# Performance work log

Measured on AMD Instinct MI355X. Metric: run time of the kernel, lower is better.

## Reference

```python
import jax, jax.numpy as jnp
import numpy as np

INNER_R = 1.0  # args.r * 0.5
OUTER_R = 2.0  # args.r
AXIS = jnp.array([[0, 0, 1], [0, 0, -1], [0, 1, 0], [0, -1, 0], [1, 0, 0], [-1, 0, 0]],
                 dtype=jnp.float32).T  # (3, 6)


def _cos2(xyz):
    # squared clipped cosine of each point direction vs 6 axes
    norm = jnp.linalg.norm(xyz, axis=-1)               # (B, N)
    cos = jnp.maximum(xyz @ AXIS, 0.0) / (norm[..., None] + 1e-8)
    return cos * cos, norm                              # (B, N, 6), (B, N)


def aggregate(direction, xyz, inner_r, outer_r):
    B, N, D6 = direction.shape
    D = D6 // 6
    cos, norm = _cos2(xyz)
    dw = 1.0 - (norm ** 2 - inner_r ** 2) / (outer_r ** 2 - inner_r ** 2)
    dw = jnp.where(dw < 0, 0.0, dw)
    dw = jnp.where(norm <= 0, 0.0, dw)
    dw = dw / jnp.sum(dw, axis=-1, keepdims=True)       # normalize over N
    cos = cos * dw[..., None]                           # (B, N, 6)
    d = direction.reshape(B, N, D, 6) * cos[:, :, None, :]
    return d.sum(axis=(1, 3))                           # sum over axes then points -> (B, D)


def disperse(signal, xyz):
    B, N, D6 = signal.shape
    D = D6 // 6
    cos, _ = _cos2(xyz)
    return (signal.reshape(B, N, D, 6) * cos[:, :, None, :]).sum(axis=-1)  # (B, N, D)


def batchnorm(x, gamma, beta, eps=1e-5):
    # training-mode BN over leading (sample) dim, biased variance like torch
    m = jnp.mean(x, axis=0)
    v = jnp.var(x, axis=0)
    return (x - m) / jnp.sqrt(v + eps) * gamma + beta


def setup_inputs() -> dict:
    key = jax.random.key(0)
    ks = jax.random.split(key, 10)
    B, N, DIM, ENC, MID, VL = 64, 2048, 10, 256, 64, 128
    s = 0.05
    p = lambda k, sh: jax.random.normal(k, sh, dtype=jnp.float32) * s
    x = jax.random.uniform(ks[0], (B, N, DIM), dtype=jnp.float32)  # xyz in [0,1) keeps points inside outer radius
    return {
        "x": x,
        "Wc": p(ks[1], (ENC, DIM)), "bc": jnp.zeros((ENC,), jnp.float32),
        "Wdir": p(ks[2], (MID * 6, DIM)),
        "g1": jnp.ones((MID,), jnp.float32), "b1": jnp.zeros((MID,), jnp.float32),
        "Wdir2": p(ks[3], (ENC, MID)),
        "g2": jnp.ones((ENC,), jnp.float32), "b2": jnp.zeros((ENC,), jnp.float32),
        "Wf1": p(ks[4], (VL, ENC)), "bf1": jnp.zeros((VL,), jnp.float32),
        "Wcm": p(ks[5], (MID, VL + 3)), "bcm": jnp.zeros((MID,), jnp.float32),
        "Wdc": p(ks[6], (ENC * 6, VL + 3)),
        "Wm0": p(ks[7], (MID, ENC)),
        "g3": jnp.ones((MID,), jnp.float32), "b3": jnp.zeros((MID,), jnp.float32),
        "Wf2": p(ks[8], (DIM - 3, MID)), "bf2": jnp.zeros((DIM - 3,), jnp.float32),
    }


def reference(x, Wc, bc, Wdir, g1, b1, Wdir2, g2, b2, Wf1, bf1,
              Wcm, bcm, Wdc, Wm0, g3, b3, Wf2, bf2):
    B, N, C = x.shape
    xyz = x[:, :, :3]
    points = x[:, :, 3:]

    # ---- GeoConv (encode) ----
    center_in = jnp.concatenate([points[:, 0, :], xyz[:, 0, :]], axis=-1)
    center = center_in @ Wc.T + bc  # computed but unused (matches torch: last_bn applied to direction only)
    dir_in = jnp.concatenate([points, xyz], axis=-1)     # (B, N, C)
    direction = dir_in @ Wdir.T                          # (B, N, mid*6)
    direction = aggregate(direction, xyz, INNER_R, OUTER_R)  # (B, mid)
    direction = jax.nn.relu(batchnorm(direction, g1, b1))
    direction = direction @ Wdir2.T                      # (B, enc_out)
    enc = jax.nn.relu(batchnorm(direction, g2, b2))
    z = enc @ Wf1.T + bf1                                # (B, vector_length)

    # ---- GeoDeConv (decode) ----
    c_in = jnp.concatenate([z, xyz[:, 0, :]], axis=-1)
    center2 = c_in @ Wcm.T + bcm                         # (B, mid)
    VL = z.shape[-1]
    sig = jnp.concatenate([xyz, jnp.broadcast_to(z[:, None, :], (B, N, VL))], axis=-1)
    sig = sig @ Wdc.T                                    # (B, N, enc_out*6)
    sig = disperse(sig, xyz)                             # (B, N, enc_out)
    sig = sig @ Wm0.T                                    # (B, N, mid)
    sig = sig.at[:, 0, :].set(center2)                   # inject center signal
    sig = jax.nn.relu(batchnorm(sig.reshape(B * N, -1), g3, b3)).reshape(B, N, -1)

    y = jax.nn.sigmoid(sig @ Wf2.T + bf2)                # (B, N, dim-3)
    return y
```

## Files before the change

kernel.cpp:

```cpp
#include <hip/hip_runtime.h>
#include <math.h>

#define BATCH 64
#define NPTS  2048
#define OFF_M    0
#define OFF_T2   4096
#define OFF_GP2  5248
#define OFF_V    8192
#define OFF_WF1T 57344
#define OFF_D2P  90112
#define OFF_C2   114688
#define OFF_U2   118784
#define OFF_MOM  143360

__global__ __launch_bounds__(256) void k_wa(const float* __restrict__ x,
                                            const float* __restrict__ Wm0,
                                            const float* __restrict__ Wdc,
                                            const float* __restrict__ Wf1,
                                            float* __restrict__ ws) {
    __shared__ __attribute__((aligned(16))) float L[61 * 257];
    int blk = blockIdx.x, t = threadIdx.x;
    if (blk < 24) {
        float* wml = L;
        float* pl  = L + 2112;
        int a = blk >> 2, vq = blk & 3;
        int m = t & 63, vg = t >> 6;
        float acc[8];
#pragma unroll
        for (int i = 0; i < 8; ++i) acc[i] = 0.f;
        for (int e0 = 0; e0 < 256; e0 += 32) {
            for (int g = t; g < 2048; g += 256)
                wml[(g >> 5) * 33 + (g & 31)] = Wm0[(g >> 5) * 256 + e0 + (g & 31)];
            for (int g = t; g < 1024; g += 256)
                pl[(g >> 5) * 36 + (g & 31)] =
                    Wdc[((e0 + (g >> 5)) * 6 + a) * 131 + 3 + vq * 32 + (g & 31)];
            __syncthreads();
#pragma unroll
            for (int e = 0; e < 32; ++e) {
                float wv = wml[m * 33 + e];
                const float4* p4 = (const float4*)(pl + e * 36 + vg * 8);
                float4 pa = p4[0], pb = p4[1];
                acc[0] = fmaf(wv, pa.x, acc[0]); acc[1] = fmaf(wv, pa.y, acc[1]);
                acc[2] = fmaf(wv, pa.z, acc[2]); acc[3] = fmaf(wv, pa.w, acc[3]);
                acc[4] = fmaf(wv, pb.x, acc[4]); acc[5] = fmaf(wv, pb.y, acc[5]);
                acc[6] = fmaf(wv, pb.z, acc[6]); acc[7] = fmaf(wv, pb.w, acc[7]);
            }
            __syncthreads();
        }
#pragma unroll
        for (int vv = 0; vv < 8; ++vv)
            ws[OFF_V + (vq * 32 + vg * 8 + vv) * 384 + m * 6 + a] = acc[vv];
    } else if (blk < 42) {
        float* col = L;
        float* red = L + 256;
        int p = blk - 24, a = p / 3, j = p % 3;
        col[t] = Wdc[(t * 6 + a) * 131 + j];
        __syncthreads();
        int m = t >> 2, q = t & 3;
        const float* wm = Wm0 + m * 256 + q * 64;
        const float* cl = col + q * 64;
        float s = 0.f;
#pragma unroll 8
        for (int i = 0; i < 64; ++i) s = fmaf(wm[i], cl[i], s);
        red[t] = s;
        __syncthreads();
        if (t < 64) {
            float v = (red[t * 4] + red[t * 4 + 1]) + (red[t * 4 + 2] + red[t * 4 + 3]);
            ws[OFF_T2 + t * 18 + a * 3 + j] = v;
        }
    } else if (blk < 106) {
        int b = blk - 42;
        float* red = L;
        float acc[61];
#pragma unroll
        for (int i = 0; i < 61; ++i) acc[i] = 0.f;
#pragma unroll 2
        for (int k = 0; k < 8; ++k) {
            int n = t + 256 * k;
            const float* xp = x + (size_t)(b * NPTS + n) * 10;
            float xv[10];
#pragma unroll
            for (int j = 0; j < 5; ++j) {
                float2 v = *(const float2*)(xp + 2 * j);
                xv[2 * j] = v.x; xv[2 * j + 1] = v.y;
            }
            float x0 = xv[0], x1 = xv[1], x2 = xv[2];
            float rn = x0 * x0 + x1 * x1 + x2 * x2;
            float norm = sqrtf(rn);
            float inv = 1.f / (norm + 1e-8f);
            float c2[6];
            c2[0] = fmaxf(x2, 0.f) * inv; c2[1] = fmaxf(-x2, 0.f) * inv;
            c2[2] = fmaxf(x1, 0.f) * inv; c2[3] = fmaxf(-x1, 0.f) * inv;
            c2[4] = fmaxf(x0, 0.f) * inv; c2[5] = fmaxf(-x0, 0.f) * inv;
#pragma unroll
            for (int a = 0; a < 6; ++a) c2[a] *= c2[a];
            float dw = 1.f - (rn - 1.f) * (1.f / 3.f);
            if (dw < 0.f) dw = 0.f;
            if (norm <= 0.f) dw = 0.f;
            float cw[6];
#pragma unroll
            for (int a = 0; a < 6; ++a) cw[a] = c2[a] * dw;
#pragma unroll
            for (int c = 0; c < 10; ++c) {
                float dv = (c < 7) ? xv[3 + c] : xv[c - 7];
#pragma unroll
                for (int a = 0; a < 6; ++a)
                    acc[c * 6 + a] = fmaf(dv, cw[a], acc[c * 6 + a]);
            }
            acc[60] += dw;
        }
#pragma unroll
        for (int i = 0; i < 61; ++i) red[i * 257 + t] = acc[i];
        __syncthreads();
        if (t < 61) {
            float s = 0.f;
#pragma unroll 8
            for (int j = 0; j < 256; ++j) s += red[t * 257 + j];
            ws[OFF_M + b * 61 + t] = s;
        }
    } else if (blk == 106) {
        if (t < 128) ws[OFF_GP2 + t] = 0.f;
    } else if (blk < 115) {
        float* slab = L;
        int w = blk - 107, v0 = w * 16;
        for (int g = t; g < 4096; g += 256)
            slab[(g >> 8) * 257 + (g & 255)] = Wf1[(v0 + (g >> 8)) * 256 + (g & 255)];
        __syncthreads();
        for (int g = t; g < 4096; g += 256) {
            int e = g >> 4, vl = g & 15;
            ws[OFF_WF1T + e * 128 + v0 + vl] = slab[vl * 257 + e];
        }
    } else if (blk < 179) {
        int b = blk - 115;
        float* red = L;
        float acc[126];
#pragma unroll
        for (int i = 0; i < 126; ++i) acc[i] = 0.f;
        for (int k = 0; k < 8; ++k) {
            int n = t + 256 * k;
            const float* xp = x + (size_t)(b * NPTS + n) * 10;
            float x0 = xp[0], x1 = xp[1], x2 = xp[2];
            float rn = x0 * x0 + x1 * x1 + x2 * x2;
            float inv = 1.f / (sqrtf(rn) + 1e-8f);
            float c[6];
            c[0] = fmaxf(x2, 0.f) * inv; c[1] = fmaxf(-x2, 0.f) * inv;
            c[2] = fmaxf(x1, 0.f) * inv; c[3] = fmaxf(-x1, 0.f) * inv;
            c[4] = fmaxf(x0, 0.f) * inv; c[5] = fmaxf(-x0, 0.f) * inv;
#pragma unroll
            for (int a = 0; a < 6; ++a) c[a] *= c[a];
            float xx[6] = {x0 * x0, x0 * x1, x0 * x2, x1 * x1, x1 * x2, x2 * x2};
#pragma unroll
            for (int a = 0; a < 6; ++a)
#pragma unroll
                for (int a2 = a; a2 < 6; ++a2) {
                    int p = a * 6 - (a * (a - 1)) / 2 + (a2 - a);
                    float cc = c[a] * c[a2];
#pragma unroll
                    for (int q = 0; q < 6; ++q)
                        acc[p * 6 + q] = fmaf(cc, xx[q], acc[p * 6 + q]);
                }
        }
#pragma unroll
        for (int i = 0; i < 61; ++i) red[i * 257 + t] = acc[i];
        __syncthreads();
        if (t < 61) {
            float s = 0.f;
#pragma unroll 8
            for (int j = 0; j < 256; ++j) s += red[t * 257 + j];
            ws[OFF_MOM + b * 240 + 108 + t] = s;
        }
        __syncthreads();
#pragma unroll
        for (int i = 0; i < 61; ++i) red[i * 257 + t] = acc[61 + i];
        __syncthreads();
        if (t < 61) {
            float s = 0.f;
#pragma unroll 8
            for (int j = 0; j < 256; ++j) s += red[t * 257 + j];
            ws[OFF_MOM + b * 240 + 108 + 61 + t] = s;
        }
        __syncthreads();
#pragma unroll
        for (int i = 0; i < 4; ++i) red[i * 257 + t] = acc[122 + i];
        __syncthreads();
        if (t < 4) {
            float s = 0.f;
#pragma unroll 8
            for (int j = 0; j < 256; ++j) s += red[t * 257 + j];
            ws[OFF_MOM + b * 240 + 108 + 122 + t] = s;
        }
    } else {
        int b = blk - 179;
        float* red = L;
        float acc[108];
#pragma unroll
        for (int i = 0; i < 108; ++i) acc[i] = 0.f;
        for (int k = 0; k < 8; ++k) {
            int n = t + 256 * k;
            const float* xp = x + (size_t)(b * NPTS + n) * 10;
            float x0 = xp[0], x1 = xp[1], x2 = xp[2];
            float rn = x0 * x0 + x1 * x1 + x2 * x2;
            float inv = 1.f / (sqrtf(rn) + 1e-8f);
            float c[6];
            c[0] = fmaxf(x2, 0.f) * inv; c[1] = fmaxf(-x2, 0.f) * inv;
            c[2] = fmaxf(x1, 0.f) * inv; c[3] = fmaxf(-x1, 0.f) * inv;
            c[4] = fmaxf(x0, 0.f) * inv; c[5] = fmaxf(-x0, 0.f) * inv;
#pragma unroll
            for (int a = 0; a < 6; ++a) c[a] *= c[a];
#pragma unroll
            for (int a = 0; a < 6; ++a) {
                acc[a] += c[a];
                acc[6 + a * 3 + 0] = fmaf(c[a], x0, acc[6 + a * 3 + 0]);
                acc[6 + a * 3 + 1] = fmaf(c[a], x1, acc[6 + a * 3 + 1]);
                acc[6 + a * 3 + 2] = fmaf(c[a], x2, acc[6 + a * 3 + 2]);
            }
#pragma unroll
            for (int a = 0; a < 6; ++a)
#pragma unroll
                for (int a2 = a; a2 < 6; ++a2) {
                    int p = a * 6 - (a * (a - 1)) / 2 + (a2 - a);
                    float cc = c[a] * c[a2];
                    acc[24 + p] += cc;
                    acc[45 + p * 3 + 0] = fmaf(cc, x0, acc[45 + p * 3 + 0]);
                    acc[45 + p * 3 + 1] = fmaf(cc, x1, acc[45 + p * 3 + 1]);
                    acc[45 + p * 3 + 2] = fmaf(cc, x2, acc[45 + p * 3 + 2]);
                }
        }
#pragma unroll
        for (int i = 0; i < 61; ++i) red[i * 257 + t] = acc[i];
        __syncthreads();
        if (t < 61) {
            float s = 0.f;
#pragma unroll 8
            for (int j = 0; j < 256; ++j) s += red[t * 257 + j];
            ws[OFF_MOM + b * 240 + t] = s;
        }
        __syncthreads();
#pragma unroll
        for (int i = 0; i < 47; ++i) red[i * 257 + t] = acc[61 + i];
        __syncthreads();
        if (t < 47) {
            float s = 0.f;
#pragma unroll 8
            for (int j = 0; j < 256; ++j) s += red[t * 257 + j];
            ws[OFF_MOM + b * 240 + 61 + t] = s;
        }
    }
}

__global__ __launch_bounds__(256) void k_d2(const float* __restrict__ Wdir,
                                            const float* __restrict__ g1,
                                            const float* __restrict__ b1,
                                            const float* __restrict__ Wdir2,
                                            const float* __restrict__ g2,
                                            const float* __restrict__ b2,
                                            float* __restrict__ ws) {
    __shared__ float L[12704];
    float* Wd  = L;
    float* Ml  = L + 3904;
    float* h1  = L + 7808;
    float* wt2 = L + 11968;
    float* d2l = L + 12228;
    float* sc  = L + 12548;
    float* of  = L + 12612;
    float* scl = L + 12676;
    float* ofl = L + 12680;
    int blk = blockIdx.x, t = threadIdx.x;
    int e_base = blk * 4;
    for (int g = t; g < 64 * 61; g += 256) Ml[g] = ws[OFF_M + g];
    for (int g = t; g < 3840; g += 256) Wd[(g / 60) * 61 + g % 60] = Wdir[g];
    if (t < 256) {
        int el = t >> 6, mm = t & 63;
        wt2[el * 65 + mm] = Wdir2[(e_base + el) * 64 + mm];
    }
    __syncthreads();
    int m = t & 63;
    float Wr[60];
#pragma unroll
    for (int r = 0; r < 60; ++r) Wr[r] = Wd[m * 61 + r];
#pragma unroll
    for (int k = 0; k < 16; ++k) {
        int idx = t + 256 * k;
        int b = idx >> 6;
        const float* Mb = Ml + b * 61;
        float s = 0.f;
#pragma unroll
        for (int a = 0; a < 6; ++a)
#pragma unroll
            for (int c = 0; c < 10; ++c)
                s = fmaf(Wr[a * 10 + c], Mb[c * 6 + a], s);
        h1[b * 65 + m] = s / Mb[60];
    }
    __syncthreads();
    if (t < 64) {
        float s = 0.f, q = 0.f;
#pragma unroll 8
        for (int b = 0; b < 64; ++b) { float v = h1[b * 65 + t]; s += v; q = fmaf(v, v, q); }
        float mean = s * (1.f / 64.f);
        float var = q * (1.f / 64.f) - mean * mean;
        float scale = g1[t] * rsqrtf(var + 1e-5f);
        sc[t] = scale; of[t] = b1[t] - mean * scale;
    }
    __syncthreads();
#pragma unroll
    for (int k = 0; k < 16; ++k) {
        int idx = t + 256 * k;
        int b = idx >> 6;
        h1[b * 65 + m] = fmaxf(fmaf(h1[b * 65 + m], sc[m], of[m]), 0.f);
    }
    __syncthreads();
    {
        int b = t >> 2, el = t & 3;
        const float* h = h1 + b * 65;
        const float* w = wt2 + el * 65;
        float s = 0.f;
#pragma unroll
        for (int mm = 0; mm < 64; ++mm) s = fmaf(h[mm], w[mm], s);
        d2l[b * 5 + el] = s;
    }
    __syncthreads();
    if (t < 4) {
        float s = 0.f, q = 0.f;
#pragma unroll 8
        for (int b = 0; b < 64; ++b) { float v = d2l[b * 5 + t]; s += v; q = fmaf(v, v, q); }
        float mean = s * (1.f / 64.f);
        float var = q * (1.f / 64.f) - mean * mean;
        int E = e_base + t;
        float scale = g2[E] * rsqrtf(var + 1e-5f);
        scl[t] = scale; ofl[t] = b2[E] - mean * scale;
    }
    __syncthreads();
    {
        int b = t >> 2, el = t & 3;
        float v = fmaxf(fmaf(d2l[b * 5 + el], scl[el], ofl[el]), 0.f);
        ws[OFF_D2P + b * 256 + e_base + el] = v;
    }
}

__global__ __launch_bounds__(512) void k_z(const float* __restrict__ x,
                                           const float* __restrict__ bf1,
                                           const float* __restrict__ Wcm,
                                           const float* __restrict__ bcm,
                                           float* __restrict__ ws) {
    __shared__ float L[11252];
    float* d2row = L;
    float* T2l   = L + 256;
    float* zp    = L + 1408;
    float* zl    = L + 1920;
    float* U2l   = L + 2048;
    float* C2l   = L + 2432;
    float* mom   = L + 2496;
    float* x0l   = L + 2736;
    float* wl    = L + 2740;
    int b = blockIdx.x, t = threadIdx.x;
    if (t < 256) d2row[t] = ws[OFF_D2P + b * 256 + t];
    for (int g = t; g < 1152; g += 512) T2l[g] = ws[OFF_T2 + g];
    if (t < 234) mom[t] = ws[OFF_MOM + b * 240 + t];
    if (t < 3) x0l[t] = x[(size_t)b * NPTS * 10 + t];
    for (int g = t; g < 8384; g += 512) wl[(g / 131) * 133 + g % 131] = Wcm[g];
    __syncthreads();
    {
        int q = t >> 7, v = t & 127;
        const float* Wt = ws + OFF_WF1T + (q * 64) * 128 + v;
        const float* d = d2row + q * 64;
        float s = 0.f;
#pragma unroll 8
        for (int e = 0; e < 64; ++e) s = fmaf(d[e], Wt[e * 128], s);
        zp[q * 128 + v] = s;
    }
    __syncthreads();
    if (t < 128)
        zl[t] = bf1[t] + ((zp[t] + zp[128 + t]) + (zp[256 + t] + zp[384 + t]));
    __syncthreads();
    if (t < 384) {
        const float* Vt = ws + OFF_V;
        float s0 = 0.f;
#pragma unroll 8
        for (int v = 0; v < 128; ++v) s0 = fmaf(zl[v], Vt[v * 384 + t], s0);
        U2l[t] = s0;
        ws[OFF_U2 + b * 384 + t] = s0;
    } else if (t < 448) {
        int m = t - 384;
        const float* w = wl + m * 133;
        float s = bcm[m];
#pragma unroll 4
        for (int i = 0; i < 128; ++i) s = fmaf(zl[i], w[i], s);
        s = fmaf(x0l[0], w[128], s);
        s = fmaf(x0l[1], w[129], s);
        s = fmaf(x0l[2], w[130], s);
        ws[OFF_C2 + b * 64 + m] = s;
        C2l[m] = s;
    }
    __syncthreads();
    if (t < 64) {
        int m = t;
        float T[18], U[6];
#pragma unroll
        for (int r = 0; r < 18; ++r) T[r] = T2l[m * 18 + r];
#pragma unroll
        for (int a = 0; a < 6; ++a) U[a] = U2l[m * 6 + a];
        float S = 0.f;
#pragma unroll
        for (int a = 0; a < 6; ++a) {
            S = fmaf(mom[6 + a * 3 + 0], T[a * 3 + 0], S);
            S = fmaf(mom[6 + a * 3 + 1], T[a * 3 + 1], S);
            S = fmaf(mom[6 + a * 3 + 2], T[a * 3 + 2], S);
            S = fmaf(mom[a], U[a], S);
        }
        float qd = 0.f, qo = 0.f;
#pragma unroll
        for (int a = 0; a < 6; ++a)
#pragma unroll
            for (int a2 = a; a2 < 6; ++a2) {
                int p = a * 6 - (a * (a - 1)) / 2 + (a2 - a);
                const float* b3 = mom + 108 + p * 6;
                const float* b2 = mom + 45 + p * 3;
                float b1v = mom[24 + p];
                float Ta0 = T[a * 3], Ta1 = T[a * 3 + 1], Ta2 = T[a * 3 + 2];
                float Tb0 = T[a2 * 3], Tb1 = T[a2 * 3 + 1], Tb2 = T[a2 * 3 + 2];
                float w0 = b3[0] * Ta0 + b3[1] * Ta1 + b3[2] * Ta2;
                float w1 = b3[1] * Ta0 + b3[3] * Ta1 + b3[4] * Ta2;
                float w2 = b3[2] * Ta0 + b3[4] * Ta1 + b3[5] * Ta2;
                float term = w0 * Tb0 + w1 * Tb1 + w2 * Tb2;
                float d1 = b2[0] * Ta0 + b2[1] * Ta1 + b2[2] * Ta2;
                float d2_ = b2[0] * Tb0 + b2[1] * Tb1 + b2[2] * Tb2;
                term += U[a2] * d1 + U[a] * d2_ + U[a] * U[a2] * b1v;
                if (a == a2) qd += term; else qo += term;
            }
        float Q = qd + 2.f * qo;
        float xx0 = x0l[0], xx1 = x0l[1], xx2 = x0l[2];
        float rn = xx0 * xx0 + xx1 * xx1 + xx2 * xx2;
        float inv = 1.f / (sqrtf(rn) + 1e-8f);
        float c2[6];
        c2[0] = fmaxf(xx2, 0.f) * inv; c2[1] = fmaxf(-xx2, 0.f) * inv;
        c2[2] = fmaxf(xx1, 0.f) * inv; c2[3] = fmaxf(-xx1, 0.f) * inv;
        c2[4] = fmaxf(xx0, 0.f) * inv; c2[5] = fmaxf(-xx0, 0.f) * inv;
        float h0 = 0.f;
#pragma unroll
        for (int a = 0; a < 6; ++a) {
            float cc = c2[a] * c2[a];
            float ta = fmaf(xx0, T[a * 3], fmaf(xx1, T[a * 3 + 1], fmaf(xx2, T[a * 3 + 2], U[a])));
            h0 = fmaf(cc, ta, h0);
        }
        float C2v = C2l[m];
        S += C2v - h0;
        Q += C2v * C2v - h0 * h0;
        atomicAdd(&ws[OFF_GP2 + m], S);
        atomicAdd(&ws[OFF_GP2 + 64 + m], Q);
    }
}

__global__ __launch_bounds__(512) void k_e(const float* __restrict__ x,
                                           const float* __restrict__ g3,
                                           const float* __restrict__ b3,
                                           const float* __restrict__ Wf2,
                                           const float* __restrict__ bf2,
                                           const float* __restrict__ ws,
                                           float* __restrict__ out) {
    __shared__ __attribute__((aligned(16))) float L[6464];
    float* Wl24 = L;
    float* Pl   = L + 1536;
    float* C2l  = L + 2304;
    float* yp   = L + 2368;
    int blk = blockIdx.x, t = threadIdx.x;
    int b = blk >> 3;
    for (int g = t; g < 1152; g += 512) {
        int m = g / 18, r = g % 18, a = r / 3, j = r % 3;
        Wl24[m * 24 + a * 4 + j] = ws[OFF_T2 + g];
    }
    if (t < 384)
        Wl24[(t / 6) * 24 + (t % 6) * 4 + 3] = ws[OFF_U2 + b * 384 + t];
    if (t < 448) {
        int m = t / 7, k = t % 7;
        Pl[m * 12 + k] = Wf2[k * 64 + m];
    }
    if (t < 64) {
        float S = ws[OFF_GP2 + t];
        float Q = ws[OFF_GP2 + 64 + t];
        float mean = S * (1.f / 131072.f);
        float var = Q * (1.f / 131072.f) - mean * mean;
        float scale = g3[t] * rsqrtf(var + 1e-5f);
        Pl[t * 12 + 7] = scale;
        Pl[t * 12 + 8] = b3[t] - mean * scale;
    }
    if ((blk & 7) == 0 && t < 64) C2l[t] = ws[OFF_C2 + b * 64 + t];
    __syncthreads();

    int p_loc = t >> 1, mh = t & 1;
    int p = blk * 256 + p_loc;
    const float* xp = x + (size_t)p * 10;
    float x0 = xp[0], x1 = xp[1], x2 = xp[2];
    float rn = x0 * x0 + x1 * x1 + x2 * x2;
    float inv = 1.f / (sqrtf(rn) + 1e-8f);
    float c2[6];
    c2[0] = fmaxf(x2, 0.f) * inv; c2[1] = fmaxf(-x2, 0.f) * inv;
    c2[2] = fmaxf(x1, 0.f) * inv; c2[3] = fmaxf(-x1, 0.f) * inv;
    c2[4] = fmaxf(x0, 0.f) * inv; c2[5] = fmaxf(-x0, 0.f) * inv;
#pragma unroll
    for (int a = 0; a < 6; ++a) c2[a] *= c2[a];
    bool c0 = ((p & 2047) == 0);
    float y[7];
#pragma unroll
    for (int k = 0; k < 7; ++k) y[k] = mh ? 0.f : bf2[k];
    int m0 = mh * 32;
#pragma unroll 4
    for (int mm = 0; mm < 32; ++mm) {
        int m = m0 + mm;
        const float4* Wm = (const float4*)(Wl24 + m * 24);
        float h = 0.f;
#pragma unroll
        for (int a = 0; a < 6; ++a) {
            float4 wq = Wm[a];
            float ta = fmaf(x0, wq.x, fmaf(x1, wq.y, fmaf(x2, wq.z, wq.w)));
            h = fmaf(c2[a], ta, h);
        }
        if (c0) h = C2l[m];
        const float4* Pm = (const float4*)(Pl + m * 12);
        float4 p0 = Pm[0], p1 = Pm[1];
        float offv = Pl[m * 12 + 8];
        float r = fmaxf(fmaf(h, p1.w, offv), 0.f);
        y[0] = fmaf(r, p0.x, y[0]); y[1] = fmaf(r, p0.y, y[1]);
        y[2] = fmaf(r, p0.z, y[2]); y[3] = fmaf(r, p0.w, y[3]);
        y[4] = fmaf(r, p1.x, y[4]); y[5] = fmaf(r, p1.y, y[5]);
        y[6] = fmaf(r, p1.z, y[6]);
    }
#pragma unroll
    for (int k = 0; k < 7; ++k) yp[p_loc * 16 + mh * 8 + k] = y[k];
    __syncthreads();
    float* op = out + (size_t)blk * 1792;
    for (int g = t; g < 1792; g += 512) {
        int pp = g / 7, k = g % 7;
        float v = yp[pp * 16 + k] + yp[pp * 16 + 8 + k];
        op[g] = 1.f / (1.f + __expf(-v));
    }
}

extern "C" void kernel_launch(void* const* d_in, const int* in_sizes, int n_in,
                              void* d_out, int out_size, void* d_ws, size_t ws_size,
                              hipStream_t stream) {
    const float* x     = (const float*)d_in[0];
    const float* Wdir  = (const float*)d_in[3];
    const float* g1    = (const float*)d_in[4];
    const float* b1    = (const float*)d_in[5];
    const float* Wdir2 = (const float*)d_in[6];
    const float* g2    = (const float*)d_in[7];
    const float* b2    = (const float*)d_in[8];
    const float* Wf1   = (const float*)d_in[9];
    const float* bf1   = (const float*)d_in[10];
    const float* Wcm   = (const float*)d_in[11];
    const float* bcm   = (const float*)d_in[12];
    const float* Wdc   = (const float*)d_in[13];
    const float* Wm0   = (const float*)d_in[14];
    const float* g3    = (const float*)d_in[15];
    const float* b3    = (const float*)d_in[16];
    const float* Wf2   = (const float*)d_in[17];
    const float* bf2   = (const float*)d_in[18];
    float* ws  = (float*)d_ws;
    float* out = (float*)d_out;

    k_wa <<<243, 256, 0, stream>>>(x, Wm0, Wdc, Wf1, ws);
    k_d2 <<<64,  256, 0, stream>>>(Wdir, g1, b1, Wdir2, g2, b2, ws);
    k_z  <<<64,  512, 0, stream>>>(x, bf1, Wcm, bcm, ws);
    k_e  <<<512, 512, 0, stream>>>(x, g3, b3, Wf2, bf2, ws, out);
}
```

Before: 165.5 us.

## Fuse k_d2 and k_z into one kernel with redundant per-block BN recompute

Merges the encoder-direction/batchnorm kernel and the latent/center kernel into a single k_mid launch of 64 blocks. Each block now recomputes the full h1 and all 256 d2 columns, including the batch statistics for both batchnorms, rather than splitting columns across blocks and exchanging them through global memory. This removes one kernel launch and the global round-trip of the d2 intermediate. The cost is 64x redundant computation of the small direction MLP and its batchnorm statistics inside each block.

Measured after the change: 199.3 us. +20.5%, slower.

```diff
diff --git a/kernel.cpp b/kernel.cpp
--- a/kernel.cpp
+++ b/kernel.cpp
@@ -8,7 +8,6 @@
 #define OFF_GP2  5248
 #define OFF_V    8192
 #define OFF_WF1T 57344
-#define OFF_D2P  90112
 #define OFF_C2   114688
 #define OFF_U2   118784
 #define OFF_MOM  143360
@@ -248,54 +247,68 @@
     }
 }
 
-__global__ __launch_bounds__(256) void k_d2(const float* __restrict__ Wdir,
-                                            const float* __restrict__ g1,
-                                            const float* __restrict__ b1,
-                                            const float* __restrict__ Wdir2,
-                                            const float* __restrict__ g2,
-                                            const float* __restrict__ b2,
-                                            float* __restrict__ ws) {
-    __shared__ float L[12704];
-    float* Wd  = L;
-    float* Ml  = L + 3904;
-    float* h1  = L + 7808;
-    float* wt2 = L + 11968;
-    float* d2l = L + 12228;
-    float* sc  = L + 12548;
-    float* of  = L + 12612;
-    float* scl = L + 12676;
-    float* ofl = L + 12680;
-    int blk = blockIdx.x, t = threadIdx.x;
-    int e_base = blk * 4;
-    for (int g = t; g < 64 * 61; g += 256) Ml[g] = ws[OFF_M + g];
-    for (int g = t; g < 3840; g += 256) Wd[(g / 60) * 61 + g % 60] = Wdir[g];
-    if (t < 256) {
-        int el = t >> 6, mm = t & 63;
-        wt2[el * 65 + mm] = Wdir2[(e_base + el) * 64 + mm];
-    }
-    __syncthreads();
+__global__ __launch_bounds__(512) void k_mid(const float* __restrict__ x,
+                                             const float* __restrict__ Wdir,
+                                             const float* __restrict__ g1,
+                                             const float* __restrict__ b1,
+                                             const float* __restrict__ Wdir2,
+                                             const float* __restrict__ g2,
+                                             const float* __restrict__ b2,
+                                             const float* __restrict__ bf1,
+                                             const float* __restrict__ Wcm,
+                                             const float* __restrict__ bcm,
+                                             float* __restrict__ ws) {
+    __shared__ __attribute__((aligned(16))) float L[14900];
+    float* Ml    = L;
+    float* Wd    = L + 3904;
+    float* w2c   = L;
+    float* d2c   = L + 3904;
+    float* h1    = L + 7808;
+    float* wcm   = L;
+    float* d2row = L + 11968;
+    float* T2l   = L + 12224;
+    float* mom   = L + 13376;
+    float* x0l   = L + 13616;
+    float* zl    = L + 13620;
+    float* zp    = L + 13748;
+    float* U2l   = L + 14260;
+    float* C2l   = L + 14644;
+    float* sc    = L + 14708;
+    float* of    = L + 14772;
+    float* scl   = L + 14836;
+    float* ofl   = L + 14868;
+    int b = blockIdx.x, t = threadIdx.x;
+
+    for (int g = t; g < 3904; g += 512) Ml[g] = ws[OFF_M + g];
+    for (int g = t; g < 3840; g += 512) Wd[(g / 60) * 61 + g % 60] = Wdir[g];
+    for (int g = t; g < 1152; g += 512) T2l[g] = ws[OFF_T2 + g];
+    if (t < 234) mom[t] = ws[OFF_MOM + b * 240 + t];
+    if (t < 3) x0l[t] = x[(size_t)b * NPTS * 10 + t];
+    __syncthreads();
+
     int m = t & 63;
     float Wr[60];
 #pragma unroll
     for (int r = 0; r < 60; ++r) Wr[r] = Wd[m * 61 + r];
 #pragma unroll
-    for (int k = 0; k < 16; ++k) {
-        int idx = t + 256 * k;
-        int b = idx >> 6;
-        const float* Mb = Ml + b * 61;
+    for (int k = 0; k < 8; ++k) {
+        int idx = t + 512 * k;
+        int bb = idx >> 6;
+        const float* Mb = Ml + bb * 61;
         float s = 0.f;
 #pragma unroll
         for (int a = 0; a < 6; ++a)
 #pragma unroll
             for (int c = 0; c < 10; ++c)
                 s = fmaf(Wr[a * 10 + c], Mb[c * 6 + a], s);
-        h1[b * 65 + m] = s / Mb[60];
-    }
-    __syncthreads();
+        h1[bb * 65 + m] = s / Mb[60];
+    }
+    __syncthreads();
+
     if (t < 64) {
         float s = 0.f, q = 0.f;
 #pragma unroll 8
-        for (int b = 0; b < 64; ++b) { float v = h1[b * 65 + t]; s += v; q = fmaf(v, v, q); }
+        for (int bb = 0; bb < 64; ++bb) { float v = h1[bb * 65 + t]; s += v; q = fmaf(v, v, q); }
         float mean = s * (1.f / 64.f);
         float var = q * (1.f / 64.f) - mean * mean;
         float scale = g1[t] * rsqrtf(var + 1e-5f);
@@ -303,62 +316,45 @@
     }
     __syncthreads();
 #pragma unroll
-    for (int k = 0; k < 16; ++k) {
-        int idx = t + 256 * k;
-        int b = idx >> 6;
-        h1[b * 65 + m] = fmaxf(fmaf(h1[b * 65 + m], sc[m], of[m]), 0.f);
-    }
-    __syncthreads();
-    {
-        int b = t >> 2, el = t & 3;
-        const float* h = h1 + b * 65;
-        const float* w = wt2 + el * 65;
-        float s = 0.f;
-#pragma unroll
-        for (int mm = 0; mm < 64; ++mm) s = fmaf(h[mm], w[mm], s);
-        d2l[b * 5 + el] = s;
-    }
-    __syncthreads();
-    if (t < 4) {
-        float s = 0.f, q = 0.f;
-#pragma unroll 8
-        for (int b = 0; b < 64; ++b) { float v = d2l[b * 5 + t]; s += v; q = fmaf(v, v, q); }
-        float mean = s * (1.f / 64.f);
-        float var = q * (1.f / 64.f) - mean * mean;
-        int E = e_base + t;
-        float scale = g2[E] * rsqrtf(var + 1e-5f);
-        scl[t] = scale; ofl[t] = b2[E] - mean * scale;
-    }
-    __syncthreads();
-    {
-        int b = t >> 2, el = t & 3;
-        float v = fmaxf(fmaf(d2l[b * 5 + el], scl[el], ofl[el]), 0.f);
-        ws[OFF_D2P + b * 256 + e_base + el] = v;
-    }
-}
-
-__global__ __launch_bounds__(512) void k_z(const float* __restrict__ x,
-                                           const float* __restrict__ bf1,
-                                           const float* __restrict__ Wcm,
-                                           const float* __restrict__ bcm,
-                                           float* __restrict__ ws) {
-    __shared__ float L[11252];
-    float* d2row = L;
-    float* T2l   = L + 256;
-    float* zp    = L + 1408;
-    float* zl    = L + 1920;
-    float* U2l   = L + 2048;
-    float* C2l   = L + 2432;
-    float* mom   = L + 2496;
-    float* x0l   = L + 2736;
-    float* wl    = L + 2740;
-    int b = blockIdx.x, t = threadIdx.x;
-    if (t < 256) d2row[t] = ws[OFF_D2P + b * 256 + t];
-    for (int g = t; g < 1152; g += 512) T2l[g] = ws[OFF_T2 + g];
-    if (t < 234) mom[t] = ws[OFF_MOM + b * 240 + t];
-    if (t < 3) x0l[t] = x[(size_t)b * NPTS * 10 + t];
-    for (int g = t; g < 8384; g += 512) wl[(g / 131) * 133 + g % 131] = Wcm[g];
-    __syncthreads();
+    for (int k = 0; k < 8; ++k) {
+        int idx = t + 512 * k;
+        int bb = idx >> 6;
+        h1[bb * 65 + m] = fmaxf(fmaf(h1[bb * 65 + m], sc[m], of[m]), 0.f);
+    }
+    __syncthreads();
+
+    for (int c8 = 0; c8 < 8; ++c8) {
+        int e_base = c8 * 32;
+        for (int g = t; g < 2048; g += 512)
+            w2c[(g >> 6) * 65 + (g & 63)] = Wdir2[(e_base + (g >> 6)) * 64 + (g & 63)];
+        __syncthreads();
+#pragma unroll
+        for (int i = 0; i < 4; ++i) {
+            int idx = t + 512 * i;
+            int bb = idx >> 5, el = idx & 31;
+            const float* h = h1 + bb * 65;
+            const float* w = w2c + el * 65;
+            float s = 0.f;
+#pragma unroll
+            for (int mm = 0; mm < 64; ++mm) s = fmaf(h[mm], w[mm], s);
+            d2c[bb * 33 + el] = s;
+        }
+        __syncthreads();
+        if (t < 32) {
+            float s = 0.f, q = 0.f;
+#pragma unroll 8
+            for (int bb = 0; bb < 64; ++bb) { float v = d2c[bb * 33 + t]; s += v; q = fmaf(v, v, q); }
+            float mean = s * (1.f / 64.f);
+            float var = q * (1.f / 64.f) - mean * mean;
+            int E = e_base + t;
+            float scale = g2[E] * rsqrtf(var + 1e-5f);
+            float off = b2[E] - mean * scale;
+            d2row[E] = fmaxf(fmaf(d2c[b * 33 + t], scale, off), 0.f);
+        }
+        __syncthreads();
+    }
+
+    for (int g = t; g < 8384; g += 512) wcm[(g / 131) * 133 + g % 131] = Wcm[g];
     {
         int q = t >> 7, v = t & 127;
         const float* Wt = ws + OFF_WF1T + (q * 64) * 128 + v;
@@ -372,6 +368,7 @@
     if (t < 128)
         zl[t] = bf1[t] + ((zp[t] + zp[128 + t]) + (zp[256 + t] + zp[384 + t]));
     __syncthreads();
+
     if (t < 384) {
         const float* Vt = ws + OFF_V;
         float s0 = 0.f;
@@ -380,25 +377,26 @@
         U2l[t] = s0;
         ws[OFF_U2 + b * 384 + t] = s0;
     } else if (t < 448) {
-        int m = t - 384;
-        const float* w = wl + m * 133;
-        float s = bcm[m];
+        int mm = t - 384;
+        const float* w = wcm + mm * 133;
+        float s = bcm[mm];
 #pragma unroll 4
         for (int i = 0; i < 128; ++i) s = fmaf(zl[i], w[i], s);
         s = fmaf(x0l[0], w[128], s);
         s = fmaf(x0l[1], w[129], s);
         s = fmaf(x0l[2], w[130], s);
-        ws[OFF_C2 + b * 64 + m] = s;
-        C2l[m] = s;
-    }
-    __syncthreads();
+        ws[OFF_C2 + b * 64 + mm] = s;
+        C2l[mm] = s;
+    }
+    __syncthreads();
+
     if (t < 64) {
-        int m = t;
+        int mm = t;
         float T[18], U[6];
 #pragma unroll
-        for (int r = 0; r < 18; ++r) T[r] = T2l[m * 18 + r];
-#pragma unroll
-        for (int a = 0; a < 6; ++a) U[a] = U2l[m * 6 + a];
+        for (int r = 0; r < 18; ++r) T[r] = T2l[mm * 18 + r];
+#pragma unroll
+        for (int a = 0; a < 6; ++a) U[a] = U2l[mm * 6 + a];
         float S = 0.f;
 #pragma unroll
         for (int a = 0; a < 6; ++a) {
@@ -414,7 +412,7 @@
             for (int a2 = a; a2 < 6; ++a2) {
                 int p = a * 6 - (a * (a - 1)) / 2 + (a2 - a);
                 const float* b3 = mom + 108 + p * 6;
-                const float* b2 = mom + 45 + p * 3;
+                const float* b2m = mom + 45 + p * 3;
                 float b1v = mom[24 + p];
                 float Ta0 = T[a * 3], Ta1 = T[a * 3 + 1], Ta2 = T[a * 3 + 2];
                 float Tb0 = T[a2 * 3], Tb1 = T[a2 * 3 + 1], Tb2 = T[a2 * 3 + 2];
@@ -422,8 +420,8 @@
                 float w1 = b3[1] * Ta0 + b3[3] * Ta1 + b3[4] * Ta2;
                 float w2 = b3[2] * Ta0 + b3[4] * Ta1 + b3[5] * Ta2;
                 float term = w0 * Tb0 + w1 * Tb1 + w2 * Tb2;
-                float d1 = b2[0] * Ta0 + b2[1] * Ta1 + b2[2] * Ta2;
-                float d2_ = b2[0] * Tb0 + b2[1] * Tb1 + b2[2] * Tb2;
+                float d1 = b2m[0] * Ta0 + b2m[1] * Ta1 + b2m[2] * Ta2;
+                float d2_ = b2m[0] * Tb0 + b2m[1] * Tb1 + b2m[2] * Tb2;
                 term += U[a2] * d1 + U[a] * d2_ + U[a] * U[a2] * b1v;
                 if (a == a2) qd += term; else qo += term;
             }
@@ -442,11 +440,11 @@
             float ta = fmaf(xx0, T[a * 3], fmaf(xx1, T[a * 3 + 1], fmaf(xx2, T[a * 3 + 2], U[a])));
             h0 = fmaf(cc, ta, h0);
         }
-        float C2v = C2l[m];
+        float C2v = C2l[mm];
         S += C2v - h0;
         Q += C2v * C2v - h0 * h0;
-        atomicAdd(&ws[OFF_GP2 + m], S);
-        atomicAdd(&ws[OFF_GP2 + 64 + m], Q);
+        atomicAdd(&ws[OFF_GP2 + mm], S);
+        atomicAdd(&ws[OFF_GP2 + 64 + mm], Q);
     }
 }
 
@@ -559,7 +557,6 @@
     float* out = (float*)d_out;
 
     k_wa <<<243, 256, 0, stream>>>(x, Wm0, Wdc, Wf1, ws);
-    k_d2 <<<64,  256, 0, stream>>>(Wdir, g1, b1, Wdir2, g2, b2, ws);
-    k_z  <<<64,  512, 0, stream>>>(x, bf1, Wcm, bcm, ws);
+    k_mid<<<64,  512, 0, stream>>>(x, Wdir, g1, b1, Wdir2, g2, b2, bf1, Wcm, bcm, ws);
     k_e  <<<512, 512, 0, stream>>>(x, g3, b3, Wf2, bf2, ws, out);
 }
```
